# Kernel tuning notes

Hardware: AMD Instinct MI355X
Metric: run time of the kernel (lower is better)

Reference implementation:

```python
import jax, jax.numpy as jnp
import numpy as np
import math

B, S, L, D, H, F = 4, 1024, 4, 256, 8, 1024
NUM_LETTERS = 22
VOCAB = NUM_LETTERS + 3
HD = D // H
DISSONANCE = 0.5


def setup_inputs() -> dict:
    key = jax.random.key(0)
    ks = iter(jax.random.split(key, 64))
    r = lambda shape, s=0.05: jax.random.normal(next(ks), shape, dtype=jnp.float32) * s
    inp = {
        'input_roots': jax.random.randint(next(ks), (B, S, 3), 0, VOCAB),
        'gematria': jax.random.uniform(next(ks), (B, S), dtype=jnp.float32),
        'letter_embed': r((VOCAB, D), 0.02),
        'root_proj_w': r((3 * D, D)), 'root_proj_b': jnp.zeros((D,)),
        'root_ln_g': jnp.ones((D,)), 'root_ln_b': jnp.zeros((D,)),
        'input_proj_w': r((2 * D, D)), 'input_proj_b': jnp.zeros((D,)),
        'input_ln_g': jnp.ones((D,)), 'input_ln_b': jnp.zeros((D,)),
        'qw': r((L, D, D)), 'qb': jnp.zeros((L, D)),
        'kw': r((L, D, D)), 'kb': jnp.zeros((L, D)),
        'vw': r((L, D, D)), 'vb': jnp.zeros((L, D)),
        'ow': r((L, D, D)), 'ob': jnp.zeros((L, D)),
        'dist_scale': r((L, H), 0.1), 'diss_sens': jnp.full((L, H), 0.5),
        'ff1w': r((L, D, F)), 'ff1b': jnp.zeros((L, F)),
        'ff2w': r((L, F, D)), 'ff2b': jnp.zeros((L, D)),
        'ln1g': jnp.ones((L, D)), 'ln1b': jnp.zeros((L, D)),
        'ln2g': jnp.ones((L, D)), 'ln2b': jnp.zeros((L, D)),
        'out_ln_g': jnp.ones((D,)), 'out_ln_b': jnp.zeros((D,)),
        'h1w': r((D, NUM_LETTERS)), 'h1b': jnp.zeros((NUM_LETTERS,)),
        'h2w': r((D, NUM_LETTERS)), 'h2b': jnp.zeros((NUM_LETTERS,)),
        'h3w': r((D, NUM_LETTERS)), 'h3b': jnp.zeros((NUM_LETTERS,)),
    }
    return inp


def _ln(x, g, b):
    m = jnp.mean(x, -1, keepdims=True)
    v = jnp.mean(jnp.square(x - m), -1, keepdims=True)
    return (x - m) * jax.lax.rsqrt(v + 1e-5) * g + b


def _rtl_pos(s, d):
    # flipped sinusoidal PE: token j gets original position s-1-j
    pos = (s - 1 - jnp.arange(s, dtype=jnp.float32))[:, None]
    div = jnp.exp(jnp.arange(0, d, 2, dtype=jnp.float32) * (-(math.log(10000.0) / d)))
    pe = jnp.zeros((s, d))
    pe = pe.at[:, 0::2].set(jnp.sin(pos * div))
    pe = pe.at[:, 1::2].set(jnp.cos(pos * div))
    return pe


def _forward(input_roots, gematria, letter_embed, root_proj_w, root_proj_b,
             root_ln_g, root_ln_b, input_proj_w, input_proj_b, input_ln_g, input_ln_b,
             qw, qb, kw, kb, vw, vb, ow, ob, dist_scale, diss_sens,
             ff1w, ff1b, ff2w, ff2b, ln1g, ln1b, ln2g, ln2b,
             out_ln_g, out_ln_b, h1w, h1b, h2w, h2b, h3w, h3b):
    b, s, _ = input_roots.shape
    # root encoder
    letters = letter_embed[input_roots]                      # (b,s,3,D)
    root_emb = _ln(letters.reshape(b, s, 3 * D) @ root_proj_w + root_proj_b, root_ln_g, root_ln_b)
    # gematria sinusoidal
    angles = (gematria[..., None] * 500.0) * jnp.exp(
        jnp.arange(0, D, 2, dtype=jnp.float32) * (-(math.log(10000.0) / D)))
    gem_emb = jnp.concatenate([jnp.sin(angles), jnp.cos(angles)], axis=-1)  # (b,s,D)
    x = jnp.concatenate([root_emb, gem_emb], axis=-1) @ input_proj_w + input_proj_b
    x = _ln(x + _rtl_pos(s, D)[None], input_ln_g, input_ln_b)
    # distance matrix |i-j| shared across layers
    pos = jnp.arange(s, dtype=jnp.float32)
    dist = jnp.abs(pos[None, :] - pos[:, None])              # (s,s)
    scale = 1.0 / math.sqrt(HD)
    for i in range(L):
        normed = _ln(x, ln1g[i], ln1b[i])
        Q = (normed @ qw[i] + qb[i]).reshape(b, s, H, HD)
        K = (normed @ kw[i] + kb[i]).reshape(b, s, H, HD)
        V = (normed @ vw[i] + vb[i]).reshape(b, s, H, HD)
        scores = jnp.einsum('bqhd,bkhd->bhqk', Q, K) * scale
        penalty = dist_scale[i] * (1.0 - DISSONANCE * diss_sens[i])  # (H,)
        bias = -jnp.abs(penalty)[:, None, None] * dist[None]         # (H,s,s)
        attn = jax.nn.softmax(scores + bias[None], axis=-1)
        out = jnp.einsum('bhqk,bkhd->bqhd', attn, V).reshape(b, s, D)
        x = x + (out @ ow[i] + ob[i])
        h = _ln(x, ln2g[i], ln2b[i])
        x = x + (jax.nn.gelu(h @ ff1w[i] + ff1b[i], approximate=False) @ ff2w[i] + ff2b[i])
    x = _ln(x, out_ln_g, out_ln_b)
    return (x @ h1w + h1b, x @ h2w + h2b, x @ h3w + h3b)


def reference(input_roots, gematria, letter_embed, root_proj_w, root_proj_b,
              root_ln_g, root_ln_b, input_proj_w, input_proj_b, input_ln_g, input_ln_b,
              qw, qb, kw, kb, vw, vb, ow, ob, dist_scale, diss_sens,
              ff1w, ff1b, ff2w, ff2b, ln1g, ln1b, ln2g, ln2b,
              out_ln_g, out_ln_b, h1w, h1b, h2w, h2b, h3w, h3b):
    return _forward(input_roots, gematria, letter_embed, root_proj_w, root_proj_b,
                    root_ln_g, root_ln_b, input_proj_w, input_proj_b, input_ln_g, input_ln_b,
                    qw, qb, kw, kb, vw, vb, ow, ob, dist_scale, diss_sens,
                    ff1w, ff1b, ff2w, ff2b, ln1g, ln1b, ln2g, ln2b,
                    out_ln_g, out_ln_b, h1w, h1b, h2w, h2b, h3w, h3b)
```

## Files before the change

### kernel.cpp

```cpp
#include <hip/hip_runtime.h>
#include <hip/hip_bf16.h>
#include <math.h>

#define NTOK   4096
#define SEQ    1024
#define DMODEL 256
#define NHEAD  8
#define FDIM   1024
#define NLAYER 4

typedef __attribute__((ext_vector_type(8))) short short8v;
typedef __attribute__((ext_vector_type(4))) float f32x4;

#define LDS3(p) ((__attribute__((address_space(3))) unsigned int*)(p))
#define GAS1(p) ((const __attribute__((address_space(1))) unsigned int*)(p))

__device__ __forceinline__ void gl_lds16(const void* g, void* l) {
    __builtin_amdgcn_global_load_lds(GAS1(g), LDS3(l), 16, 0, 0);
}
__device__ __forceinline__ short f2bf(float v) {
    __hip_bfloat16 h = __float2bfloat16(v);
    return __builtin_bit_cast(short, h);
}

struct TD { const float* src; __hip_bfloat16* dst; int K; int M; int Mpad; };
struct TDs { TD d[29]; };

__global__ __launch_bounds__(256) void transpose_kernel(TDs p) {
    __shared__ float ld[32][33];
    TD d = p.d[blockIdx.y];
    int tm = (d.Mpad + 31) >> 5;
    int kt = blockIdx.x / tm, mt = blockIdx.x % tm;
    if (kt * 32 >= d.K) return;
    int tx = threadIdx.x & 31, ty = threadIdx.x >> 5;
    #pragma unroll
    for (int r = 0; r < 4; ++r) {
        int k = kt * 32 + ty + r * 8, m = mt * 32 + tx;
        if (m < d.M) ld[ty + r * 8][tx] = d.src[(long)k * d.M + m];
    }
    __syncthreads();
    #pragma unroll
    for (int r = 0; r < 4; ++r) {
        int m = mt * 32 + ty + r * 8, k = kt * 32 + tx;
        if (m < d.M) d.dst[(long)m * d.K + k] = __float2bfloat16(ld[tx][ty + r * 8]);
        else if (m < d.Mpad) d.dst[(long)m * d.K + k] = __float2bfloat16(0.f);
    }
}

template <int TM, int TN, int EPI>
__global__ __launch_bounds__(256) void mm_kernel(
    const __hip_bfloat16* __restrict__ A, const __hip_bfloat16* __restrict__ Bw,
    const float* __restrict__ bias, float* __restrict__ Cf,
    __hip_bfloat16* __restrict__ Cb, int N, int K, int M,
    const float* __restrict__ b2, const float* __restrict__ b3,
    __hip_bfloat16* __restrict__ Ck, __hip_bfloat16* __restrict__ Cv)
{
    constexpr int BK = 64;
    __shared__ __align__(16) short As[2][TM * BK];
    __shared__ __align__(16) short Bs[2][TN * BK];
    const int tid = threadIdx.x;
    const int lane = tid & 63, wid = tid >> 6;
    const int wr = wid >> 1, wc = wid & 1;
    const int n0 = blockIdx.y * TM, m0 = blockIdx.x * TN;
    const int l15 = lane & 15, g = lane >> 4;
    constexpr int FM = (TM / 32 > 0) ? TM / 32 : 1;
    constexpr int FN = TN / 32;
    f32x4 acc[FM][FN] = {};
    const int nt = K >> 6;

    auto stage = [&](int buf, int k0) {
        constexpr int CA = TM * 8;
        #pragma unroll
        for (int j = 0; j < (CA + 255) / 256; ++j) {
            int cid = tid + j * 256;
            if (CA % 256 == 0 || cid < CA) {
                int r = cid >> 3, sl = cid & 7, ss = sl ^ (r & 7);
                gl_lds16(A + (long)(n0 + r) * K + k0 + ss * 8, (char*)As[buf] + cid * 16);
            }
        }
        constexpr int CB = TN * 8;
        #pragma unroll
        for (int j = 0; j < CB / 256; ++j) {
            int cid = tid + j * 256;
            int r = cid >> 3, sl = cid & 7, ss = sl ^ (r & 7);
            gl_lds16(Bw + (long)(m0 + r) * K + k0 + ss * 8, (char*)Bs[buf] + cid * 16);
        }
    };

    stage(0, 0);
    __syncthreads();
    for (int t = 0; t < nt; ++t) {
        int cur = t & 1;
        if (t + 1 < nt) stage(cur ^ 1, (t + 1) * BK);
        #pragma unroll
        for (int ks = 0; ks < 2; ++ks) {
            short8v af[FM], bfr[FN];
            #pragma unroll
            for (int mi = 0; mi < FM; ++mi) {
                int row = wr * (TM / 2) + mi * 16 + l15;
                int slot = (ks * 4 + g) ^ (row & 7);
                af[mi] = *(const short8v*)((const char*)As[cur] + row * (BK * 2) + slot * 16);
            }
            #pragma unroll
            for (int ni = 0; ni < FN; ++ni) {
                int row = wc * (TN / 2) + ni * 16 + l15;
                int slot = (ks * 4 + g) ^ (row & 7);
                bfr[ni] = *(const short8v*)((const char*)Bs[cur] + row * (BK * 2) + slot * 16);
            }
            #pragma unroll
            for (int mi = 0; mi < FM; ++mi)
                #pragma unroll
                for (int ni = 0; ni < FN; ++ni)
                    acc[mi][ni] = __builtin_amdgcn_mfma_f32_16x16x32_bf16(
                        af[mi], bfr[ni], acc[mi][ni], 0, 0, 0);
        }
        __syncthreads();
    }

    #pragma unroll
    for (int mi = 0; mi < FM; ++mi) {
        #pragma unroll
        for (int ni = 0; ni < FN; ++ni) {
            int colb = m0 + wc * (TN / 2) + ni * 16 + l15;
            float bv;
            if (EPI == 6) bv = (colb < 256) ? bias[colb] : (colb < 512) ? b2[colb - 256] : b3[colb - 512];
            else bv = bias[colb];
            if (EPI == 6 && colb >= 512) {
                int c2 = colb - 512;
                int h = c2 >> 5, dd = c2 & 31;
                int row0 = n0 + wr * (TM / 2) + mi * 16 + g * 4;
                int bb = row0 >> 10, ss = row0 & 1023;
                short4 pk;
                pk.x = f2bf(acc[mi][ni][0] + bv);
                pk.y = f2bf(acc[mi][ni][1] + bv);
                pk.z = f2bf(acc[mi][ni][2] + bv);
                pk.w = f2bf(acc[mi][ni][3] + bv);
                *(short4*)((short*)Cv + ((long)((bb * 8 + h) * 32 + dd) << 10) + ss) = pk;
            } else {
                #pragma unroll
                for (int i = 0; i < 4; ++i) {
                    int row = n0 + wr * (TM / 2) + mi * 16 + g * 4 + i;
                    float v = acc[mi][ni][i] + bv;
                    if (EPI == 0) Cf[(long)row * M + colb] = v;
                    else if (EPI == 2) {
                        v = 0.5f * v * (1.f + erff(v * 0.70710678f));
                        Cb[(long)row * M + colb] = __float2bfloat16(v);
                    } else if (EPI == 5) {
                        if (colb < 66) {
                            int hd = colb / 22, jj = colb - hd * 22;
                            Cf[(long)hd * (NTOK * 22) + (long)row * 22 + jj] = v;
                        }
                    } else if (EPI == 6) {
                        __hip_bfloat16* dst = (colb < 256) ? Cb : Ck;
                        int cc = (colb < 256) ? colb : colb - 256;
                        dst[(long)row * 256 + cc] = __float2bfloat16(v);
                    }
                }
            }
        }
    }
}

#define WIDE_GEMM_BODY(Abuf, Bwp, Kval)                                           \
    constexpr int BK = 64;                                                        \
    const int tid = threadIdx.x;                                                  \
    const int lane = tid & 63, wid = tid >> 6;                                    \
    const int l15 = lane & 15, g = lane >> 4;                                     \
    const int n0 = blockIdx.x * 16;                                               \
    f32x4 acc[4] = {};                                                            \
    const int nt = (Kval) >> 6;                                                   \
    auto stage = [&](int buf, int k0) {                                           \
        if (tid < 128) {                                                          \
            int r = tid >> 3, sl = tid & 7, ss = sl ^ (r & 7);                    \
            gl_lds16((Abuf) + (long)(n0 + r) * (Kval) + k0 + ss * 8,              \
                     (char*)As[buf] + tid * 16);                                  \
        }                                                                         \
        _Pragma("unroll")                                                         \
        for (int j = 0; j < 8; ++j) {                                             \
            int cid = tid + j * 256;                                              \
            int r = cid >> 3, sl = cid & 7, ss = sl ^ (r & 7);                    \
            gl_lds16((Bwp) + (long)r * (Kval) + k0 + ss * 8,                      \
                     (char*)Bs[buf] + cid * 16);                                  \
        }                                                                         \
    };                                                                            \
    stage(0, 0);                                                                  \
    __syncthreads();                                                              \
    for (int t = 0; t < nt; ++t) {                                                \
        int cur = t & 1;                                                          \
        if (t + 1 < nt) stage(cur ^ 1, (t + 1) * BK);                             \
        _Pragma("unroll")                                                         \
        for (int ks = 0; ks < 2; ++ks) {                                          \
            short8v af;                                                           \
            {                                                                     \
                int slot = (ks * 4 + g) ^ (l15 & 7);                              \
                af = *(const short8v*)((const char*)As[cur] + l15 * (BK * 2) + slot * 16); \
            }                                                                     \
            _Pragma("unroll")                                                     \
            for (int ni = 0; ni < 4; ++ni) {                                      \
                int brow = wid * 64 + ni * 16 + l15;                              \
                int slot = (ks * 4 + g) ^ (brow & 7);                             \
                short8v bfr = *(const short8v*)((const char*)Bs[cur] + brow * (BK * 2) + slot * 16); \
                acc[ni] = __builtin_amdgcn_mfma_f32_16x16x32_bf16(af, bfr, acc[ni], 0, 0, 0); \
            }                                                                     \
        }                                                                         \
        __syncthreads();                                                          \
    }

__device__ __forceinline__ void wide_rowstats(
    float pvt[4][4], float2 red2[4][16], int wid, int l15, int g,
    float mean[4], float rstd[4])
{
    float rs[4] = {0.f, 0.f, 0.f, 0.f}, rq[4] = {0.f, 0.f, 0.f, 0.f};
    #pragma unroll
    for (int ni = 0; ni < 4; ++ni)
        #pragma unroll
        for (int i = 0; i < 4; ++i) { rs[i] += pvt[ni][i]; rq[i] += pvt[ni][i] * pvt[ni][i]; }
    #pragma unroll
    for (int i = 0; i < 4; ++i) {
        #pragma unroll
        for (int off = 8; off; off >>= 1) {
            rs[i] += __shfl_xor(rs[i], off);
            rq[i] += __shfl_xor(rq[i], off);
        }
    }
    __syncthreads();
    if (l15 == 0) {
        #pragma unroll
        for (int i = 0; i < 4; ++i)
            red2[wid][g * 4 + i] = make_float2(rs[i], rq[i]);
    }
    __syncthreads();
    #pragma unroll
    for (int i = 0; i < 4; ++i) {
        int lr = g * 4 + i;
        float s1 = red2[0][lr].x + red2[1][lr].x + red2[2][lr].x + red2[3][lr].x;
        float s2 = red2[0][lr].y + red2[1][lr].y + red2[2][lr].y + red2[3][lr].y;
        float mn = s1 * (1.f / 256.f);
        float var = s2 * (1.f / 256.f) - mn * mn;
        mean[i] = mn;
        rstd[i] = rsqrtf(var + 1e-5f);
    }
}

__global__ __launch_bounds__(256) void mm_wide_ln_kernel(
    const __hip_bfloat16* __restrict__ A, const __hip_bfloat16* __restrict__ Bw,
    const float* __restrict__ bias, float* __restrict__ xio,
    __hip_bfloat16* __restrict__ nrm, const float* __restrict__ lng,
    const float* __restrict__ lnb, int K)
{
    __shared__ __align__(16) short As[2][16 * 64];
    __shared__ __align__(16) short Bs[2][256 * 64];
    __shared__ float2 red2[4][16];
    WIDE_GEMM_BODY(A, Bw, K)

    float pvt[4][4];
    #pragma unroll
    for (int ni = 0; ni < 4; ++ni) {
        int col = wid * 64 + ni * 16 + l15;
        float bv = bias[col];
        #pragma unroll
        for (int i = 0; i < 4; ++i) {
            int row = n0 + g * 4 + i;
            pvt[ni][i] = acc[ni][i] + bv + xio[(long)row * 256 + col];
        }
    }
    float mean[4], rstd[4];
    wide_rowstats(pvt, red2, wid, l15, g, mean, rstd);
    #pragma unroll
    for (int i = 0; i < 4; ++i) {
        int row = n0 + g * 4 + i;
        #pragma unroll
        for (int ni = 0; ni < 4; ++ni) {
            int col = wid * 64 + ni * 16 + l15;
            float v = pvt[ni][i];
            xio[(long)row * 256 + col] = v;
            nrm[(long)row * 256 + col] =
                __float2bfloat16((v - mean[i]) * rstd[i] * lng[col] + lnb[col]);
        }
    }
}

__global__ __launch_bounds__(256) void wide_gem_kernel(
    const __hip_bfloat16* __restrict__ A, const __hip_bfloat16* __restrict__ Bw,
    const float* __restrict__ bias, const float* __restrict__ lng,
    const float* __restrict__ lnb, const float* __restrict__ gem,
    __hip_bfloat16* __restrict__ catin)
{
    __shared__ __align__(16) short As[2][16 * 64];
    __shared__ __align__(16) short Bs[2][256 * 64];
    __shared__ float2 red2[4][16];
    WIDE_GEMM_BODY(A, Bw, 768)

    const float LC = 0.0359778921f;
    float pvt[4][4];
    #pragma unroll
    for (int ni = 0; ni < 4; ++ni) {
        int col = wid * 64 + ni * 16 + l15;
        float bv = bias[col];
        #pragma unroll
        for (int i = 0; i < 4; ++i) pvt[ni][i] = acc[ni][i] + bv;
    }
    float mean[4], rstd[4];
    wide_rowstats(pvt, red2, wid, l15, g, mean, rstd);
    float gv[4];
    #pragma unroll
    for (int i = 0; i < 4; ++i) gv[i] = gem[n0 + g * 4 + i];
    #pragma unroll
    for (int ni = 0; ni < 4; ++ni) {
        int col = wid * 64 + ni * 16 + l15;
        int j = col & 127;
        float c = 500.f * __expf(-(float)(2 * j) * LC);
        #pragma unroll
        for (int i = 0; i < 4; ++i) {
            int row = n0 + g * 4 + i;
            catin[(long)row * 512 + col] = __float2bfloat16(
                (pvt[ni][i] - mean[i]) * rstd[i] * lng[col] + lnb[col]);
            float ang = gv[i] * c;
            float gval = (col < 128) ? __sinf(ang) : __cosf(ang);
            catin[(long)row * 512 + 256 + col] = __float2bfloat16(gval);
        }
    }
}

__global__ __launch_bounds__(256) void wide_pe_kernel(
    const __hip_bfloat16* __restrict__ A, const __hip_bfloat16* __restrict__ Bw,
    const float* __restrict__ bias, const float* __restrict__ lng,
    const float* __restrict__ lnb, const float* __restrict__ g1,
    const float* __restrict__ b1, float* __restrict__ x,
    __hip_bfloat16* __restrict__ nrm)
{
    __shared__ __align__(16) short As[2][16 * 64];
    __shared__ __align__(16) short Bs[2][256 * 64];
    __shared__ float2 red2[4][16];
    WIDE_GEMM_BODY(A, Bw, 512)

    const float LC = 0.0359778921f;
    float pvt[4][4];
    #pragma unroll
    for (int ni = 0; ni < 4; ++ni) {
        int col = wid * 64 + ni * 16 + l15;
        float bv = bias[col];
        float dv = __expf(-(float)(col & ~1) * LC);
        #pragma unroll
        for (int i = 0; i < 4; ++i) {
            int row = n0 + g * 4 + i;
            float pos = (float)(1023 - (row & 1023));
            float pe = (col & 1) ? __cosf(pos * dv) : __sinf(pos * dv);
            pvt[ni][i] = acc[ni][i] + bv + pe;
        }
    }
    float mean[4], rstd[4];
    wide_rowstats(pvt, red2, wid, l15, g, mean, rstd);
    #pragma unroll
    for (int ni = 0; ni < 4; ++ni) {
        int col = wid * 64 + ni * 16 + l15;
        #pragma unroll
        for (int i = 0; i < 4; ++i) {
            float xv = (pvt[ni][i] - mean[i]) * rstd[i] * lng[col] + lnb[col];
            pvt[ni][i] = xv;
            x[(long)(n0 + g * 4 + i) * 256 + col] = xv;
        }
    }
    __syncthreads();
    wide_rowstats(pvt, red2, wid, l15, g, mean, rstd);
    #pragma unroll
    for (int ni = 0; ni < 4; ++ni) {
        int col = wid * 64 + ni * 16 + l15;
        #pragma unroll
        for (int i = 0; i < 4; ++i) {
            int row = n0 + g * 4 + i;
            nrm[(long)row * 256 + col] = __float2bfloat16(
                (pvt[ni][i] - mean[i]) * rstd[i] * g1[col] + b1[col]);
        }
    }
}

__global__ __launch_bounds__(64) void attn_mfma_kernel(
    const __hip_bfloat16* __restrict__ Q, const __hip_bfloat16* __restrict__ Kx,
    const __hip_bfloat16* __restrict__ Vt, __hip_bfloat16* __restrict__ Oa,
    const float* __restrict__ dsc, const float* __restrict__ dss)
{
    __shared__ __align__(16) short Ps[16 * 64];
    const int lane = threadIdx.x;
    const int qt = blockIdx.x;
    const int bh = blockIdx.y, b = bh >> 3, h = bh & 7;
    const int l15 = lane & 15, g = lane >> 4;
    const float pen = fabsf(dsc[h] * (1.f - 0.5f * dss[h]));
    const float scale = 0.17677669529663689f;

    short8v bq = *(const short8v*)(Q + ((long)(b * SEQ + qt * 16 + l15) * DMODEL + h * 32 + g * 8));

    float m = -1e30f, l = 0.f;
    f32x4 oacc[2] = {};
    const float qpos = (float)(qt * 16 + l15);
    char* pbase = (char*)Ps + l15 * 128;

    int klo = 0, khi = 15;
    {
        float D = 30.f / pen;
        float kmin = (float)(qt * 16) - D;
        float kmax = (float)(qt * 16 + 15) + D;
        klo = max(0, (int)floorf(kmin * (1.f / 64.f)));
        khi = min(15, (int)floorf(kmax * (1.f / 64.f)));
    }

    for (int kt = klo; kt <= khi; ++kt) {
        short8v ak[4];
        #pragma unroll
        for (int ni = 0; ni < 4; ++ni) {
            int key = kt * 64 + ni * 16 + l15;
            ak[ni] = *(const short8v*)(Kx + ((long)(b * SEQ + key) * DMODEL + h * 32 + g * 8));
        }
        short8v vb[2][2];
        #pragma unroll
        for (int ks = 0; ks < 2; ++ks)
            #pragma unroll
            for (int n2 = 0; n2 < 2; ++n2) {
                int d = n2 * 16 + l15;
                vb[ks][n2] = *(const short8v*)(Vt + ((long)(bh * 32 + d) << 10) + kt * 64 + ks * 32 + g * 8);
            }

        float s[4][4];
        float smax = -1e30f;
        #pragma unroll
        for (int ni = 0; ni < 4; ++ni) {
            f32x4 z = {0.f, 0.f, 0.f, 0.f};
            f32x4 sa = __builtin_amdgcn_mfma_f32_16x16x32_bf16(ak[ni], bq, z, 0, 0, 0);
            float kbase = (float)(kt * 64 + ni * 16 + g * 4);
            #pragma unroll
            for (int i = 0; i < 4; ++i) {
                float v = sa[i] * scale - pen * fabsf(qpos - (kbase + (float)i));
                s[ni][i] = v;
                smax = fmaxf(smax, v);
            }
        }
        smax = fmaxf(smax, __shfl_xor(smax, 16));
        smax = fmaxf(smax, __shfl_xor(smax, 32));
        float mn = fmaxf(m, smax);
        float fac = __expf(m - mn);
        m = mn;
        float ps = 0.f;
        #pragma unroll
        for (int ni = 0; ni < 4; ++ni) {
            short4 pk;
            #pragma unroll
            for (int i = 0; i < 4; ++i) {
                float p = __expf(s[ni][i] - mn);
                ps += p;
                ((short*)&pk)[i] = f2bf(p);
            }
            int slot = (ni * 2 + (g >> 1)) ^ (l15 & 7);
            *(short4*)(pbase + slot * 16 + (g & 1) * 8) = pk;
        }
        ps += __shfl_xor(ps, 16);
        ps += __shfl_xor(ps, 32);
        l = l * fac + ps;

        float facr[4];
        #pragma unroll
        for (int i = 0; i < 4; ++i) facr[i] = __shfl(fac, g * 4 + i);
        #pragma unroll
        for (int n2 = 0; n2 < 2; ++n2)
            #pragma unroll
            for (int i = 0; i < 4; ++i) oacc[n2][i] *= facr[i];

        #pragma unroll
        for (int ks = 0; ks < 2; ++ks) {
            int slot = (ks * 4 + g) ^ (l15 & 7);
            short8v pa = *(const short8v*)(pbase + slot * 16);
            #pragma unroll
            for (int n2 = 0; n2 < 2; ++n2)
                oacc[n2] = __builtin_amdgcn_mfma_f32_16x16x32_bf16(pa, vb[ks][n2], oacc[n2], 0, 0, 0);
        }
    }
    float lr[4];
    #pragma unroll
    for (int i = 0; i < 4; ++i) lr[i] = __shfl(l, g * 4 + i);
    #pragma unroll
    for (int n2 = 0; n2 < 2; ++n2) {
        #pragma unroll
        for (int i = 0; i < 4; ++i) {
            float v = oacc[n2][i] / lr[i];
            long row = b * SEQ + qt * 16 + g * 4 + i;
            Oa[row * DMODEL + h * 32 + n2 * 16 + l15] = __float2bfloat16(v);
        }
    }
}

__global__ __launch_bounds__(256) void gather_kernel(
    const int* __restrict__ roots, const float* __restrict__ letE,
    __hip_bfloat16* __restrict__ cat,
    const float* __restrict__ h1b, const float* __restrict__ h2b,
    const float* __restrict__ h3b, float* __restrict__ biascat)
{
    const int n = blockIdx.x, t = threadIdx.x;
    int r0 = roots[n * 3 + 0], r1 = roots[n * 3 + 1], r2 = roots[n * 3 + 2];
    cat[(long)n * 768 + t]       = __float2bfloat16(letE[r0 * DMODEL + t]);
    cat[(long)n * 768 + 256 + t] = __float2bfloat16(letE[r1 * DMODEL + t]);
    cat[(long)n * 768 + 512 + t] = __float2bfloat16(letE[r2 * DMODEL + t]);
    if (n == 0 && t < 66)
        biascat[t] = (t < 22) ? h1b[t] : (t < 44) ? h2b[t - 22] : h3b[t - 44];
}

extern "C" void kernel_launch(void* const* d_in, const int* in_sizes, int n_in,
                              void* d_out, int out_size, void* d_ws, size_t ws_size,
                              hipStream_t stream)
{
    const int*   roots = (const int*)  d_in[0];
    const float* gem   = (const float*)d_in[1];
    const float* letE  = (const float*)d_in[2];
    const float* rpw   = (const float*)d_in[3];
    const float* rpb   = (const float*)d_in[4];
    const float* rlg   = (const float*)d_in[5];
    const float* rlb   = (const float*)d_in[6];
    const float* ipw   = (const float*)d_in[7];
    const float* ipb   = (const float*)d_in[8];
    const float* ilg   = (const float*)d_in[9];
    const float* ilb   = (const float*)d_in[10];
    const float* qw    = (const float*)d_in[11];
    const float* qb    = (const float*)d_in[12];
    const float* kw    = (const float*)d_in[13];
    const float* kb    = (const float*)d_in[14];
    const float* vw    = (const float*)d_in[15];
    const float* vb    = (const float*)d_in[16];
    const float* ow    = (const float*)d_in[17];
    const float* ob    = (const float*)d_in[18];
    const float* dsc   = (const float*)d_in[19];
    const float* dss   = (const float*)d_in[20];
    const float* ff1w  = (const float*)d_in[21];
    const float* ff1b  = (const float*)d_in[22];
    const float* ff2w  = (const float*)d_in[23];
    const float* ff2b  = (const float*)d_in[24];
    const float* ln1g  = (const float*)d_in[25];
    const float* ln1b  = (const float*)d_in[26];
    const float* ln2g  = (const float*)d_in[27];
    const float* ln2b  = (const float*)d_in[28];
    const float* olng  = (const float*)d_in[29];
    const float* olnb  = (const float*)d_in[30];
    const float* h1w   = (const float*)d_in[31];
    const float* h1b   = (const float*)d_in[32];
    const float* h2w   = (const float*)d_in[33];
    const float* h2b   = (const float*)d_in[34];
    const float* h3w   = (const float*)d_in[35];
    const float* h3b   = (const float*)d_in[36];

    char* wsb = (char*)d_ws;
    float*          x    = (float*)         (wsb + (0l  << 20));
    __hip_bfloat16* nrm  = (__hip_bfloat16*)(wsb + (8l  << 20));
    __hip_bfloat16* qbuf = (__hip_bfloat16*)(wsb + (10l << 20));
    __hip_bfloat16* kbuf = (__hip_bfloat16*)(wsb + (12l << 20));
    __hip_bfloat16* vtb  = (__hip_bfloat16*)(wsb + (14l << 20));
    __hip_bfloat16* aob  = (__hip_bfloat16*)(wsb + (16l << 20));
    __hip_bfloat16* hbb  = (__hip_bfloat16*)(wsb + (18l << 20));
    __hip_bfloat16* catb  = hbb;
    __hip_bfloat16* catin = qbuf;
    __hip_bfloat16* wb   = (__hip_bfloat16*)(wsb + (26l << 20));
    float*          biascat = (float*)      (wsb + (34l << 20));

    __hip_bfloat16* rpw_t  = wb;
    __hip_bfloat16* ipw_t  = wb + 196608;
    __hip_bfloat16* qkv_t  = wb + 327680;
    __hip_bfloat16* ow_t   = wb + 1114112;
    __hip_bfloat16* ff1w_t = wb + 1376256;
    __hip_bfloat16* ff2w_t = wb + 2424832;
    __hip_bfloat16* head_t = wb + 3473408;

    TDs td;
    td.d[0] = {rpw, rpw_t, 768, 256, 256};
    td.d[1] = {ipw, ipw_t, 512, 256, 256};
    for (int l = 0; l < 4; ++l) {
        td.d[2 + l]  = {qw + l * 65536,  qkv_t + l * 196608 + 0,      256, 256, 256};
        td.d[6 + l]  = {kw + l * 65536,  qkv_t + l * 196608 + 65536,  256, 256, 256};
        td.d[10 + l] = {vw + l * 65536,  qkv_t + l * 196608 + 131072, 256, 256, 256};
        td.d[14 + l] = {ow + l * 65536,  ow_t + l * 65536,  256, 256, 256};
        td.d[18 + l] = {ff1w + l * 262144, ff1w_t + l * 262144, 256, 1024, 1024};
        td.d[22 + l] = {ff2w + l * 262144, ff2w_t + l * 262144, 1024, 256, 256};
    }
    td.d[26] = {h1w, head_t + 0 * 22 * 256, 256, 22, 22};
    td.d[27] = {h2w, head_t + 1 * 22 * 256, 256, 22, 22};
    td.d[28] = {h3w, head_t + 2 * 22 * 256, 256, 22, 84};
    transpose_kernel<<<dim3(256, 29), 256, 0, stream>>>(td);

    gather_kernel<<<NTOK, 256, 0, stream>>>(roots, letE, catb, h1b, h2b, h3b, biascat);
    wide_gem_kernel<<<dim3(NTOK / 16), 256, 0, stream>>>(
        catb, rpw_t, rpb, rlg, rlb, gem, catin);
    wide_pe_kernel<<<dim3(NTOK / 16), 256, 0, stream>>>(
        catin, ipw_t, ipb, ilg, ilb, ln1g, ln1b, x, nrm);

    for (int l = 0; l < NLAYER; ++l) {
        mm_kernel<64, 64, 6><<<dim3(12, 64), 256, 0, stream>>>(
            nrm, qkv_t + l * 196608, qb + l * 256, nullptr, qbuf, NTOK, 256, 768,
            kb + l * 256, vb + l * 256, kbuf, vtb);
        attn_mfma_kernel<<<dim3(64, 32), 64, 0, stream>>>(qbuf, kbuf, vtb, aob,
                                                          dsc + l * 8, dss + l * 8);
        mm_wide_ln_kernel<<<dim3(NTOK / 16), 256, 0, stream>>>(
            aob, ow_t + l * 65536, ob + l * 256, x, nrm,
            ln2g + l * 256, ln2b + l * 256, 256);
        mm_kernel<64, 64, 2><<<dim3(16, 64), 256, 0, stream>>>(
            nrm, ff1w_t + l * 262144, ff1b + l * 1024, nullptr, hbb, NTOK, 256, 1024,
            nullptr, nullptr, nullptr, nullptr);
        const float* ng = (l == 3) ? olng : ln1g + (l + 1) * 256;
        const float* nb = (l == 3) ? olnb : ln1b + (l + 1) * 256;
        mm_wide_ln_kernel<<<dim3(NTOK / 16), 256, 0, stream>>>(
            hbb, ff2w_t + l * 262144, ff2b + l * 256, x, nrm, ng, nb, 1024);
    }
    mm_kernel<32, 64, 5><<<dim3(2, 128), 256, 0, stream>>>(
        nrm, head_t, biascat, (float*)d_out, nullptr, NTOK, 256, 128,
        nullptr, nullptr, nullptr, nullptr);
}
```

Baseline: 475.8 us.

## Share K/V tiles across four query waves in attention and fuse embedding gather

The attention kernel now uses 256-thread blocks covering 64 queries. K and V tiles are double-buffered in LDS through async global-to-LDS loads and shared by four waves, instead of each 64-thread block loading them straight into registers. The separate gather kernel is removed: the root-projection GEMM gathers bf16 letter embeddings directly by root index, and the head biases are selected inside the epilogue. This is meant to cut redundant global K/V traffic and an intermediate buffer write/read, at the cost of fewer attention blocks and a wider key window per block.

```diff
diff --git a/kernel.cpp b/kernel.cpp
--- a/kernel.cpp
+++ b/kernel.cpp
@@ -8,6 +8,7 @@
 #define NHEAD  8
 #define FDIM   1024
 #define NLAYER 4
+#define VOCAB  25
 
 typedef __attribute__((ext_vector_type(8))) short short8v;
 typedef __attribute__((ext_vector_type(4))) float f32x4;
@@ -21,6 +22,13 @@
 __device__ __forceinline__ short f2bf(float v) {
     __hip_bfloat16 h = __float2bfloat16(v);
     return __builtin_bit_cast(short, h);
+}
+
+__global__ __launch_bounds__(256) void cvt_kernel(
+    const float* __restrict__ src, __hip_bfloat16* __restrict__ dst, int n)
+{
+    int i = blockIdx.x * 256 + threadIdx.x;
+    if (i < n) dst[i] = __float2bfloat16(src[i]);
 }
 
 struct TD { const float* src; __hip_bfloat16* dst; int K; int M; int Mpad; };
@@ -124,6 +132,7 @@
             int colb = m0 + wc * (TN / 2) + ni * 16 + l15;
             float bv;
             if (EPI == 6) bv = (colb < 256) ? bias[colb] : (colb < 512) ? b2[colb - 256] : b3[colb - 512];
+            else if (EPI == 5) bv = (colb < 22) ? bias[colb] : (colb < 44) ? b2[colb - 22] : (colb < 66) ? b3[colb - 44] : 0.f;
             else bv = bias[colb];
             if (EPI == 6 && colb >= 512) {
                 int c2 = colb - 512;
@@ -281,7 +290,8 @@
 }
 
 __global__ __launch_bounds__(256) void wide_gem_kernel(
-    const __hip_bfloat16* __restrict__ A, const __hip_bfloat16* __restrict__ Bw,
+    const int* __restrict__ roots, const __hip_bfloat16* __restrict__ letEbf,
+    const __hip_bfloat16* __restrict__ Bw,
     const float* __restrict__ bias, const float* __restrict__ lng,
     const float* __restrict__ lnb, const float* __restrict__ gem,
     __hip_bfloat16* __restrict__ catin)
@@ -289,7 +299,49 @@
     __shared__ __align__(16) short As[2][16 * 64];
     __shared__ __align__(16) short Bs[2][256 * 64];
     __shared__ float2 red2[4][16];
-    WIDE_GEMM_BODY(A, Bw, 768)
+    constexpr int BK = 64;
+    const int tid = threadIdx.x;
+    const int lane = tid & 63, wid = tid >> 6;
+    const int l15 = lane & 15, g = lane >> 4;
+    const int n0 = blockIdx.x * 16;
+    f32x4 acc[4] = {};
+    const int nt = 12;
+    auto stage = [&](int buf, int k0) {
+        if (tid < 128) {
+            int r = tid >> 3, sl = tid & 7, ss = sl ^ (r & 7);
+            int j = k0 >> 8, off = (k0 & 255) + ss * 8;
+            int root = roots[(n0 + r) * 3 + j];
+            gl_lds16(letEbf + (long)root * 256 + off, (char*)As[buf] + tid * 16);
+        }
+        #pragma unroll
+        for (int j = 0; j < 8; ++j) {
+            int cid = tid + j * 256;
+            int r = cid >> 3, sl = cid & 7, ss = sl ^ (r & 7);
+            gl_lds16(Bw + (long)r * 768 + k0 + ss * 8, (char*)Bs[buf] + cid * 16);
+        }
+    };
+    stage(0, 0);
+    __syncthreads();
+    for (int t = 0; t < nt; ++t) {
+        int cur = t & 1;
+        if (t + 1 < nt) stage(cur ^ 1, (t + 1) * BK);
+        #pragma unroll
+        for (int ks = 0; ks < 2; ++ks) {
+            short8v af;
+            {
+                int slot = (ks * 4 + g) ^ (l15 & 7);
+                af = *(const short8v*)((const char*)As[cur] + l15 * (BK * 2) + slot * 16);
+            }
+            #pragma unroll
+            for (int ni = 0; ni < 4; ++ni) {
+                int brow = wid * 64 + ni * 16 + l15;
+                int slot = (ks * 4 + g) ^ (brow & 7);
+                short8v bfr = *(const short8v*)((const char*)Bs[cur] + brow * (BK * 2) + slot * 16);
+                acc[ni] = __builtin_amdgcn_mfma_f32_16x16x32_bf16(af, bfr, acc[ni], 0, 0, 0);
+            }
+        }
+        __syncthreads();
+    }
 
     const float LC = 0.0359778921f;
     float pvt[4][4];
@@ -375,57 +427,72 @@
     }
 }
 
-__global__ __launch_bounds__(64) void attn_mfma_kernel(
+__global__ __launch_bounds__(256) void attn_mfma_kernel(
     const __hip_bfloat16* __restrict__ Q, const __hip_bfloat16* __restrict__ Kx,
     const __hip_bfloat16* __restrict__ Vt, __hip_bfloat16* __restrict__ Oa,
     const float* __restrict__ dsc, const float* __restrict__ dss)
 {
-    __shared__ __align__(16) short Ps[16 * 64];
-    const int lane = threadIdx.x;
-    const int qt = blockIdx.x;
-    const int bh = blockIdx.y, b = bh >> 3, h = bh & 7;
+    __shared__ __align__(16) short Qs[64 * 32];
+    __shared__ __align__(16) short Ks[2][64 * 32];
+    __shared__ __align__(16) short Vs[2][32 * 64];
+    __shared__ __align__(16) short Ps[4 * 16 * 64];
+    const int tid = threadIdx.x, lane = tid & 63, wid = tid >> 6;
+    const int qt = blockIdx.x, bh = blockIdx.y, b = bh >> 3, h = bh & 7;
+    const float pen = fabsf(dsc[h] * (1.f - 0.5f * dss[h]));
     const int l15 = lane & 15, g = lane >> 4;
-    const float pen = fabsf(dsc[h] * (1.f - 0.5f * dss[h]));
     const float scale = 0.17677669529663689f;
 
-    short8v bq = *(const short8v*)(Q + ((long)(b * SEQ + qt * 16 + l15) * DMODEL + h * 32 + g * 8));
-
-    float m = -1e30f, l = 0.f;
-    f32x4 oacc[2] = {};
-    const float qpos = (float)(qt * 16 + l15);
-    char* pbase = (char*)Ps + l15 * 128;
+    auto stageKV = [&](int buf, int kt) {
+        int r = tid >> 2, sl = tid & 3, ss = sl ^ (r & 3);
+        gl_lds16(Kx + ((long)(b * SEQ + kt * 64 + r) * DMODEL + h * 32) + ss * 8,
+                 (char*)Ks[buf] + tid * 16);
+        int d = tid >> 3, sl8 = tid & 7, ss8 = sl8 ^ (d & 7);
+        gl_lds16(Vt + ((long)(bh * 32 + d) << 10) + kt * 64 + ss8 * 8,
+                 (char*)Vs[buf] + tid * 16);
+    };
 
     int klo = 0, khi = 15;
     {
         float D = 30.f / pen;
-        float kmin = (float)(qt * 16) - D;
-        float kmax = (float)(qt * 16 + 15) + D;
+        float kmin = (float)(qt * 64) - D;
+        float kmax = (float)(qt * 64 + 63) + D;
         klo = max(0, (int)floorf(kmin * (1.f / 64.f)));
         khi = min(15, (int)floorf(kmax * (1.f / 64.f)));
     }
 
+    {
+        int r = tid >> 2, sl = tid & 3, ss = sl ^ (r & 3);
+        gl_lds16(Q + ((long)(b * SEQ + qt * 64 + r) * DMODEL + h * 32) + ss * 8,
+                 (char*)Qs + tid * 16);
+    }
+    stageKV(0, klo);
+    __syncthreads();
+
+    short8v bq;
+    {
+        int row = wid * 16 + l15;
+        int slot = g ^ (row & 3);
+        bq = *(const short8v*)((const char*)Qs + row * 64 + slot * 16);
+    }
+
+    float m = -1e30f, l = 0.f;
+    f32x4 oacc[2] = {};
+    const float qpos = (float)(qt * 64 + wid * 16 + l15);
+    char* pbase = (char*)Ps + wid * 2048 + l15 * 128;
+
     for (int kt = klo; kt <= khi; ++kt) {
-        short8v ak[4];
-        #pragma unroll
-        for (int ni = 0; ni < 4; ++ni) {
-            int key = kt * 64 + ni * 16 + l15;
-            ak[ni] = *(const short8v*)(Kx + ((long)(b * SEQ + key) * DMODEL + h * 32 + g * 8));
-        }
-        short8v vb[2][2];
-        #pragma unroll
-        for (int ks = 0; ks < 2; ++ks)
-            #pragma unroll
-            for (int n2 = 0; n2 < 2; ++n2) {
-                int d = n2 * 16 + l15;
-                vb[ks][n2] = *(const short8v*)(Vt + ((long)(bh * 32 + d) << 10) + kt * 64 + ks * 32 + g * 8);
-            }
+        int cur = (kt - klo) & 1;
+        if (kt < khi) stageKV(cur ^ 1, kt + 1);
 
         float s[4][4];
         float smax = -1e30f;
         #pragma unroll
         for (int ni = 0; ni < 4; ++ni) {
+            int krow = ni * 16 + l15;
+            int slot = g ^ (krow & 3);
+            short8v ak = *(const short8v*)((const char*)Ks[cur] + krow * 64 + slot * 16);
             f32x4 z = {0.f, 0.f, 0.f, 0.f};
-            f32x4 sa = __builtin_amdgcn_mfma_f32_16x16x32_bf16(ak[ni], bq, z, 0, 0, 0);
+            f32x4 sa = __builtin_amdgcn_mfma_f32_16x16x32_bf16(ak, bq, z, 0, 0, 0);
             float kbase = (float)(kt * 64 + ni * 16 + g * 4);
             #pragma unroll
             for (int i = 0; i < 4; ++i) {
@@ -469,9 +536,14 @@
             int slot = (ks * 4 + g) ^ (l15 & 7);
             short8v pa = *(const short8v*)(pbase + slot * 16);
             #pragma unroll
-            for (int n2 = 0; n2 < 2; ++n2)
-                oacc[n2] = __builtin_amdgcn_mfma_f32_16x16x32_bf16(pa, vb[ks][n2], oacc[n2], 0, 0, 0);
-        }
+            for (int n2 = 0; n2 < 2; ++n2) {
+                int d = n2 * 16 + l15;
+                int vslot = (ks * 4 + g) ^ (d & 7);
+                short8v vb = *(const short8v*)((const char*)Vs[cur] + d * 128 + vslot * 16);
+                oacc[n2] = __builtin_amdgcn_mfma_f32_16x16x32_bf16(pa, vb, oacc[n2], 0, 0, 0);
+            }
+        }
+        __syncthreads();
     }
     float lr[4];
     #pragma unroll
@@ -481,25 +553,10 @@
         #pragma unroll
         for (int i = 0; i < 4; ++i) {
             float v = oacc[n2][i] / lr[i];
-            long row = b * SEQ + qt * 16 + g * 4 + i;
+            long row = b * SEQ + qt * 64 + wid * 16 + g * 4 + i;
             Oa[row * DMODEL + h * 32 + n2 * 16 + l15] = __float2bfloat16(v);
         }
     }
-}
-
-__global__ __launch_bounds__(256) void gather_kernel(
-    const int* __restrict__ roots, const float* __restrict__ letE,
-    __hip_bfloat16* __restrict__ cat,
-    const float* __restrict__ h1b, const float* __restrict__ h2b,
-    const float* __restrict__ h3b, float* __restrict__ biascat)
-{
-    const int n = blockIdx.x, t = threadIdx.x;
-    int r0 = roots[n * 3 + 0], r1 = roots[n * 3 + 1], r2 = roots[n * 3 + 2];
-    cat[(long)n * 768 + t]       = __float2bfloat16(letE[r0 * DMODEL + t]);
-    cat[(long)n * 768 + 256 + t] = __float2bfloat16(letE[r1 * DMODEL + t]);
-    cat[(long)n * 768 + 512 + t] = __float2bfloat16(letE[r2 * DMODEL + t]);
-    if (n == 0 && t < 66)
-        biascat[t] = (t < 22) ? h1b[t] : (t < 44) ? h2b[t - 22] : h3b[t - 44];
 }
 
 extern "C" void kernel_launch(void* const* d_in, const int* in_sizes, int n_in,
@@ -552,10 +609,8 @@
     __hip_bfloat16* vtb  = (__hip_bfloat16*)(wsb + (14l << 20));
     __hip_bfloat16* aob  = (__hip_bfloat16*)(wsb + (16l << 20));
     __hip_bfloat16* hbb  = (__hip_bfloat16*)(wsb + (18l << 20));
-    __hip_bfloat16* catb  = hbb;
     __hip_bfloat16* catin = qbuf;
     __hip_bfloat16* wb   = (__hip_bfloat16*)(wsb + (26l << 20));
-    float*          biascat = (float*)      (wsb + (34l << 20));
 
     __hip_bfloat16* rpw_t  = wb;
     __hip_bfloat16* ipw_t  = wb + 196608;
@@ -564,6 +619,7 @@
     __hip_bfloat16* ff1w_t = wb + 1376256;
     __hip_bfloat16* ff2w_t = wb + 2424832;
     __hip_bfloat16* head_t = wb + 3473408;
+    __hip_bfloat16* letEbf = wb + 3506176;
 
     TDs td;
     td.d[0] = {rpw, rpw_t, 768, 256, 256};
@@ -580,10 +636,10 @@
     td.d[27] = {h2w, head_t + 1 * 22 * 256, 256, 22, 22};
     td.d[28] = {h3w, head_t + 2 * 22 * 256, 256, 22, 84};
     transpose_kernel<<<dim3(256, 29), 256, 0, stream>>>(td);
-
-    gather_kernel<<<NTOK, 256, 0, stream>>>(roots, letE, catb, h1b, h2b, h3b, biascat);
+    cvt_kernel<<<VOCAB, 256, 0, stream>>>(letE, letEbf, VOCAB * 256);
+
     wide_gem_kernel<<<dim3(NTOK / 16), 256, 0, stream>>>(
-        catb, rpw_t, rpb, rlg, rlb, gem, catin);
+        roots, letEbf, rpw_t, rpb, rlg, rlb, gem, catin);
     wide_pe_kernel<<<dim3(NTOK / 16), 256, 0, stream>>>(
         catin, ipw_t, ipb, ilg, ilb, ln1g, ln1b, x, nrm);
 
@@ -591,8 +647,8 @@
         mm_kernel<64, 64, 6><<<dim3(12, 64), 256, 0, stream>>>(
             nrm, qkv_t + l * 196608, qb + l * 256, nullptr, qbuf, NTOK, 256, 768,
             kb + l * 256, vb + l * 256, kbuf, vtb);
-        attn_mfma_kernel<<<dim3(64, 32), 64, 0, stream>>>(qbuf, kbuf, vtb, aob,
-                                                          dsc + l * 8, dss + l * 8);
+        attn_mfma_kernel<<<dim3(16, 32), 256, 0, stream>>>(qbuf, kbuf, vtb, aob,
+                                                           dsc + l * 8, dss + l * 8);
         mm_wide_ln_kernel<<<dim3(NTOK / 16), 256, 0, stream>>>(
             aob, ow_t + l * 65536, ob + l * 256, x, nrm,
             ln2g + l * 256, ln2b + l * 256, 256);
@@ -605,6 +661,6 @@
             hbb, ff2w_t + l * 262144, ff2b + l * 256, x, nrm, ng, nb, 1024);
     }
     mm_kernel<32, 64, 5><<<dim3(2, 128), 256, 0, stream>>>(
-        nrm, head_t, biascat, (float*)d_out, nullptr, NTOK, 256, 128,
-        nullptr, nullptr, nullptr, nullptr);
-}
+        nrm, head_t, h1b, (float*)d_out, nullptr, NTOK, 256, 128,
+        h2b, h3b, nullptr, nullptr);
+}
```

Result: faster. 418.0 us (-12.2%).
